# Kernel optimization log

Hardware: AMD Instinct MI355X
Metric: run time of the kernel (lower is better)

Reference implementation:

```python
import jax, jax.numpy as jnp
import numpy as np

N, E, DIN, H = 10000, 80000, 1024, 512
NEG = 0.2  # PyG GATv2Conv default negative_slope


def gatv2(x, src, dst, wl, bl, wr, br, att, b, n):
    # GATv2: e_ij = att . leaky_relu(Wl x_j + Wr x_i); segment softmax over dst; sum alpha * Wl x_j
    xl = x @ wl + bl            # [N, H] source transform
    xr = x @ wr + br            # [N, H] target transform
    z = jax.nn.leaky_relu(xl[src] + xr[dst], NEG)   # [E, H]
    e = z @ att                                      # [E]
    m = jax.ops.segment_max(e, dst, num_segments=n)  # per-target max (self-loops guarantee nonempty)
    p = jnp.exp(e - m[dst])
    s = jax.ops.segment_sum(p, dst, num_segments=n)
    alpha = p / (s[dst] + 1e-16)                     # [E]
    out = jax.ops.segment_sum(alpha[:, None] * xl[src], dst, num_segments=n)
    return out + b


def setup_inputs() -> dict:
    key = jax.random.key(0)
    ks = iter(jax.random.split(key, 64))
    d = {}
    d["x"] = jax.random.normal(next(ks), (N, DIN), jnp.float32)
    d["edge_index"] = jax.random.randint(next(ks), (2, E), 0, N, dtype=jnp.int32).astype(jnp.int64)
    dims = [DIN, H, H, H]
    for i in range(4):
        din = dims[i]
        sc = 1.0 / np.sqrt(din)
        d[f"wl{i+1}"] = jax.random.normal(next(ks), (din, H), jnp.float32) * sc
        d[f"bl{i+1}"] = jnp.zeros((H,), jnp.float32)
        d[f"wr{i+1}"] = jax.random.normal(next(ks), (din, H), jnp.float32) * sc
        d[f"br{i+1}"] = jnp.zeros((H,), jnp.float32)
        d[f"att{i+1}"] = jax.random.normal(next(ks), (H,), jnp.float32) * (1.0 / np.sqrt(H))
        d[f"b{i+1}"] = jnp.zeros((H,), jnp.float32)
    for name, din, dout in [("1", H, 512), ("2", 512, 256), ("3", 256, 2)]:
        d[f"lw{name}"] = jax.random.normal(next(ks), (din, dout), jnp.float32) * (1.0 / np.sqrt(din))
        d[f"lb{name}"] = jnp.zeros((dout,), jnp.float32)
    return d


def reference(x, edge_index, wl1, bl1, wr1, br1, att1, b1,
              wl2, bl2, wr2, br2, att2, b2,
              wl3, bl3, wr3, br3, att3, b3,
              wl4, bl4, wr4, br4, att4, b4,
              lw1, lb1, lw2, lb2, lw3, lb3):
    n = x.shape[0]
    loops = jnp.arange(n, dtype=edge_index.dtype)
    src = jnp.concatenate([edge_index[0], loops])  # add self-loops (PyG default)
    dst = jnp.concatenate([edge_index[1], loops])
    h = jax.nn.relu(gatv2(x, src, dst, wl1, bl1, wr1, br1, att1, b1, n))
    h = jax.nn.relu(gatv2(h, src, dst, wl2, bl2, wr2, br2, att2, b2, n))
    h = jax.nn.relu(gatv2(h, src, dst, wl3, bl3, wr3, br3, att3, b3, n))
    h = jax.nn.relu(gatv2(h, src, dst, wl4, bl4, wr4, br4, att4, b4, n))
    # dropout is identity at inference
    h = jax.nn.relu(h @ lw1 + lb1)
    h = jax.nn.relu(h @ lw2 + lb2)
    logits = h @ lw3 + lb3
    return logits, jax.nn.softmax(logits, axis=1)
```

## Files before the change

kernel.cpp:

```cpp
#include <hip/hip_runtime.h>
#include <cstdint>

#define NN 10000
#define NE 80000
#define DIN_ 1024
#define HH 512

typedef __attribute__((ext_vector_type(8))) short bf16x8;
typedef __attribute__((ext_vector_type(4))) float f32x4;
typedef unsigned short u16;
typedef unsigned int u32;

static __device__ __forceinline__ float b2f(u16 u) {
  u32 i = ((u32)u) << 16;
  return __builtin_bit_cast(float, i);
}
static __device__ __forceinline__ u16 f2b(float f) {
  u32 i = __builtin_bit_cast(u32, f);
  u32 r = (i + 0x7fffu + ((i >> 16) & 1u)) >> 16;
  return (u16)r;
}
static __device__ __forceinline__ void unpack8(uint4 u, float* f) {
  f[0] = __builtin_bit_cast(float, u.x << 16);
  f[1] = __builtin_bit_cast(float, u.x & 0xffff0000u);
  f[2] = __builtin_bit_cast(float, u.y << 16);
  f[3] = __builtin_bit_cast(float, u.y & 0xffff0000u);
  f[4] = __builtin_bit_cast(float, u.z << 16);
  f[5] = __builtin_bit_cast(float, u.z & 0xffff0000u);
  f[6] = __builtin_bit_cast(float, u.w << 16);
  f[7] = __builtin_bit_cast(float, u.w & 0xffff0000u);
}
static __device__ __forceinline__ void load8(const u16* p, float* f) { unpack8(*(const uint4*)p, f); }

#define ASYNC_CP16(gp, lp)                                                        \
  __builtin_amdgcn_global_load_lds((__attribute__((address_space(1))) void*)(gp), \
                                   (__attribute__((address_space(3))) void*)(lp), \
                                   16, 0, 0)

static __device__ __forceinline__ int float_flag(const u16* xw) {
  __shared__ int c;
  if (threadIdx.x == 0) c = 0;
  __syncthreads();
  int bad = 0;
  for (int i = threadIdx.x; i < 2048; i += blockDim.x) {
    u32 e = (xw[i] >> 7) & 0xFFu;
    if (e >= 140u) bad++;
  }
  if (bad) atomicAdd(&c, bad);
  __syncthreads();
  return c > 64;
}
static __device__ __forceinline__ int int64_flag(const u32* ew) {
  __shared__ int c;
  if (threadIdx.x == 0) c = 0;
  __syncthreads();
  int z = 0;
  for (int i = threadIdx.x; i < 256; i += blockDim.x)
    if (ew[2 * i + 1] == 0u) z++;
  if (z) atomicAdd(&c, z);
  __syncthreads();
  return c > 200;
}

__global__ void k_edges(const void* ei, int* esrc, int* edst, int* counts) {
  int f64 = int64_flag((const u32*)ei);
  int i = blockIdx.x * 256 + threadIdx.x;
  if (i < NE) {
    int sv, dv;
    if (f64) {
      sv = (int)((const long long*)ei)[i];
      dv = (int)((const long long*)ei)[NE + i];
    } else {
      sv = ((const int*)ei)[i];
      dv = ((const int*)ei)[NE + i];
    }
    esrc[i] = sv;
    edst[i] = dv;
    atomicAdd(&counts[dv], 1);
  } else if (i < NE + NN) {
    atomicAdd(&counts[i - NE], 1);
  }
}

__global__ void k_scan(const int* counts, int* rowptr, int* cursor, int n) {
  __shared__ int lds[1024];
  __shared__ int carry;
  int t = threadIdx.x;
  if (t == 0) { carry = 0; rowptr[0] = 0; }
  __syncthreads();
  for (int base = 0; base < n; base += 1024) {
    int v = (base + t < n) ? counts[base + t] : 0;
    lds[t] = v;
    __syncthreads();
    for (int off = 1; off < 1024; off <<= 1) {
      int x = (t >= off) ? lds[t - off] : 0;
      __syncthreads();
      lds[t] += x;
      __syncthreads();
    }
    if (base + t < n) {
      int inc = lds[t] + carry;
      rowptr[base + t + 1] = inc;
      cursor[base + t] = inc - v;
    }
    __syncthreads();
    if (t == 1023) carry += lds[1023];
    __syncthreads();
  }
}

__global__ void k_scatter(const int* src, const int* dst, int* cursor, int* col, int E, int n) {
  int i = blockIdx.x * blockDim.x + threadIdx.x;
  if (i < E) {
    int p = atomicAdd(&cursor[dst[i]], 1);
    col[p] = src[i];
  } else if (i < E + n) {
    int v = i - E;
    int p = atomicAdd(&cursor[v], 1);
    col[p] = v;
  }
}

struct CvtAll {
  const void* xin;
  u16* xout;
  const void* vin[20];
  u16* vout[20];
  int vn[20];
};
__global__ void k_convert(CvtAll a) {
  int f = float_flag((const u16*)a.xin);
  if (blockIdx.x < 1024) {
    for (int i = blockIdx.x * 256 + threadIdx.x; i < NN * DIN_; i += 1024 * 256)
      a.xout[i] = f ? f2b(((const float*)a.xin)[i]) : ((const u16*)a.xin)[i];
  } else {
    int v = blockIdx.x - 1024;
    const void* in = a.vin[v];
    u16* out = a.vout[v];
    int n = a.vn[v];
    for (int i = threadIdx.x; i < n; i += 256)
      out[i] = f ? f2b(((const float*)in)[i]) : ((const u16*)in)[i];
  }
}

struct TrAll {
  const void* xin;
  const void* in[10];
  u16* out[10];
  int K[10], N[10], off[10];
};
__global__ void k_trall(TrAll a) {
  __shared__ u16 tt[32][33];
  int f = float_flag((const u16*)a.xin);
  int b = blockIdx.x;
  int seg = 0;
#pragma unroll
  for (int i = 1; i < 10; i++)
    if (b >= a.off[i]) seg = i;
  int tl = b - a.off[seg];
  int K = a.K[seg], N = a.N[seg];
  int tiles_n = N >> 5;
  int n0 = (tl % tiles_n) << 5, k0 = (tl / tiles_n) << 5;
  const void* in = a.in[seg];
  u16* out = a.out[seg];
  int tx = threadIdx.x & 31, ty = threadIdx.x >> 5;
  for (int r = ty; r < 32; r += 8) {
    size_t idx = (size_t)(k0 + r) * N + n0 + tx;
    tt[r][tx] = f ? f2b(((const float*)in)[idx]) : ((const u16*)in)[idx];
  }
  __syncthreads();
  for (int r = ty; r < 32; r += 8) out[(size_t)(n0 + r) * K + k0 + tx] = tt[tx][r];
}

__global__ __launch_bounds__(256) void k_gemm128(const u16* __restrict__ A, int lda,
                                                 const u16* __restrict__ Bt,
                                                 const u16* __restrict__ bias,
                                                 u16* __restrict__ C,
                                                 int M, int N, int K, int act) {
  __shared__ u16 sA[2 * 128 * 32];
  __shared__ u16 sB[2 * 128 * 32];
  int t = threadIdx.x;
  int wave = t >> 6, lane = t & 63;
  int m0 = blockIdx.y << 7, n0 = blockIdx.x << 7;

  const u16* agp[4];
  const u16* bgp[4];
  u16* la[4];
  u16* lb[4];
#pragma unroll
  for (int q = 0; q < 4; q++) {
    int h = q >> 1;
    int row = ((q & 1) << 6) + (t >> 2);
    int kc = (t & 3) * 8;
    int ra = m0 + row;
    ra = ra < M ? ra : M - 1;
    agp[q] = A + (size_t)ra * lda + h * 32 + kc;
    bgp[q] = Bt + (size_t)(n0 + row) * K + h * 32 + kc;
    int lofs = h * 4096 + (((q & 1) << 8) + t) * 8;
    la[q] = sA + lofs;
    lb[q] = sB + lofs;
  }

  int wm = (wave >> 1) << 6, wn = (wave & 1) << 6;
  int lr = lane & 15, lko = (lane >> 4) << 3;

  f32x4 acc[4][4];
#pragma unroll
  for (int i = 0; i < 4; i++)
#pragma unroll
    for (int j = 0; j < 4; j++) acc[i][j] = (f32x4){0.f, 0.f, 0.f, 0.f};

  for (int k0 = 0; k0 < K; k0 += 64) {
#pragma unroll
    for (int q = 0; q < 4; q++) ASYNC_CP16(agp[q] + k0, la[q]);
#pragma unroll
    for (int q = 0; q < 4; q++) ASYNC_CP16(bgp[q] + k0, lb[q]);
    __syncthreads();
    bf16x8 a[2][4], b[2][4];
#pragma unroll
    for (int s = 0; s < 2; s++) {
#pragma unroll
      for (int i = 0; i < 4; i++) a[s][i] = *(const bf16x8*)(sA + s * 4096 + (wm + i * 16 + lr) * 32 + lko);
#pragma unroll
      for (int j = 0; j < 4; j++) b[s][j] = *(const bf16x8*)(sB + s * 4096 + (wn + j * 16 + lr) * 32 + lko);
    }
#pragma unroll
    for (int s = 0; s < 2; s++)
#pragma unroll
      for (int i = 0; i < 4; i++)
#pragma unroll
        for (int j = 0; j < 4; j++)
          acc[i][j] = __builtin_amdgcn_mfma_f32_16x16x32_bf16(a[s][i], b[s][j], acc[i][j], 0, 0, 0);
    __syncthreads();
  }

  int rbase = (lane >> 4) << 2;
#pragma unroll
  for (int j = 0; j < 4; j++) {
    int colc = n0 + wn + j * 16 + lr;
    float bv = b2f(bias[colc]);
#pragma unroll
    for (int i = 0; i < 4; i++) {
#pragma unroll
      for (int r = 0; r < 4; r++) {
        int row = m0 + wm + i * 16 + rbase + r;
        if (row < M) {
          float v = acc[i][j][r] + bv;
          if (act) v = fmaxf(v, 0.f);
          C[(size_t)row * N + colc] = f2b(v);
        }
      }
    }
  }
}

__global__ __launch_bounds__(256) void k_attn2(u16* __restrict__ xlr,
                                               const u16* __restrict__ att, const u16* __restrict__ bias,
                                               const int* __restrict__ rowptr, const int* __restrict__ col,
                                               int n) {
  int node = (blockIdx.x * 256 + threadIdx.x) >> 6;
  if (node >= n) return;
  int lane = threadIdx.x & 63;
  int h0 = lane * 8;
  float a[8], r[8];
  load8(att + h0, a);
  load8(xlr + (size_t)node * 1024 + 512 + h0, r);
  int e0 = rowptr[node], e1 = rowptr[node + 1];

  float m = -3e38f, s = 0.f;
  float acc[8] = {0.f, 0.f, 0.f, 0.f, 0.f, 0.f, 0.f, 0.f};
  uint4 raw = *(const uint4*)(xlr + (size_t)col[e0] * 1024 + h0);
  for (int e = e0; e < e1; e++) {
    int jn = col[(e + 1 < e1) ? e + 1 : e];
    float xv[8];
    unpack8(raw, xv);
    uint4 rawn = *(const uint4*)(xlr + (size_t)jn * 1024 + h0);
    float part = 0.f;
#pragma unroll
    for (int i = 0; i < 8; i++) {
      float z = xv[i] + r[i];
      z = z > 0.f ? z : 0.2f * z;
      part = fmaf(a[i], z, part);
    }
#pragma unroll
    for (int off = 32; off >= 1; off >>= 1) part += __shfl_xor(part, off);
    float mn = fmaxf(m, part);
    float al = __expf(m - mn);
    float w = __expf(part - mn);
    s = s * al + w;
#pragma unroll
    for (int i = 0; i < 8; i++) acc[i] = fmaf(acc[i], al, w * xv[i]);
    m = mn;
    raw = rawn;
  }
  float inv = 1.f / (s + 1e-16f);

  float bv[8];
  load8(bias + h0, bv);
  uint4 o;
  u32 p[8];
#pragma unroll
  for (int i = 0; i < 8; i++) {
    float v = fmaf(acc[i], inv, bv[i]);
    v = fmaxf(v, 0.f);
    p[i] = f2b(v);
  }
  o.x = p[0] | (p[1] << 16);
  o.y = p[2] | (p[3] << 16);
  o.z = p[4] | (p[5] << 16);
  o.w = p[6] | (p[7] << 16);
  *(uint4*)(xlr + (size_t)node * 1024 + 512 + h0) = o;
}

__global__ __launch_bounds__(256) void k_head(const u16* __restrict__ h2, const u16* __restrict__ lw3,
                                              const u16* __restrict__ lb3, float* __restrict__ out, int n) {
  int row = (blockIdx.x * 256 + threadIdx.x) >> 6;
  if (row >= n) return;
  int lane = threadIdx.x & 63;
  int k0 = lane * 4;
  uint2 hu = *(const uint2*)(h2 + (size_t)row * 256 + k0);
  float hx[4];
  hx[0] = __builtin_bit_cast(float, hu.x << 16);
  hx[1] = __builtin_bit_cast(float, hu.x & 0xffff0000u);
  hx[2] = __builtin_bit_cast(float, hu.y << 16);
  hx[3] = __builtin_bit_cast(float, hu.y & 0xffff0000u);
  float wv[8];
  load8(lw3 + (size_t)k0 * 2, wv);
  float p0 = 0.f, p1 = 0.f;
#pragma unroll
  for (int i = 0; i < 4; i++) {
    p0 = fmaf(hx[i], wv[2 * i], p0);
    p1 = fmaf(hx[i], wv[2 * i + 1], p1);
  }
#pragma unroll
  for (int off = 32; off >= 1; off >>= 1) {
    p0 += __shfl_xor(p0, off);
    p1 += __shfl_xor(p1, off);
  }
  if (lane == 0) {
    float l0 = p0 + b2f(lb3[0]);
    float l1 = p1 + b2f(lb3[1]);
    float mx = fmaxf(l0, l1);
    float q0 = __expf(l0 - mx), q1 = __expf(l1 - mx);
    float si = 1.f / (q0 + q1);
    out[row * 2 + 0] = l0;
    out[row * 2 + 1] = l1;
    out[2 * n + row * 2 + 0] = q0 * si;
    out[2 * n + row * 2 + 1] = q1 * si;
  }
}

extern "C" void kernel_launch(void* const* d_in, const int* in_sizes, int n_in,
                              void* d_out, int out_size, void* d_ws, size_t ws_size,
                              hipStream_t stream) {
  (void)in_sizes; (void)n_in; (void)out_size; (void)ws_size;
  const void* x_raw = d_in[0];
  const void* ei_raw = d_in[1];
  const void *wl[4], *bl[4], *wr[4], *br[4], *att[4], *bg[4];
  for (int i = 0; i < 4; i++) {
    wl[i] = d_in[2 + i * 6 + 0];
    bl[i] = d_in[2 + i * 6 + 1];
    wr[i] = d_in[2 + i * 6 + 2];
    br[i] = d_in[2 + i * 6 + 3];
    att[i] = d_in[2 + i * 6 + 4];
    bg[i] = d_in[2 + i * 6 + 5];
  }
  const void* lw1 = d_in[26];
  const void* lb1 = d_in[27];
  const void* lw2 = d_in[28];
  const void* lb2 = d_in[29];
  const void* lw3 = d_in[30];
  const void* lb3 = d_in[31];

  size_t off = 0;
  auto alloc = [&](size_t bytes) -> void* {
    off = (off + 255) & ~(size_t)255;
    void* p = (char*)d_ws + off;
    off += bytes;
    return p;
  };
  int* esrc = (int*)alloc(NE * 4);
  int* edst = (int*)alloc(NE * 4);
  int* counts = (int*)alloc(NN * 4);
  int* rowptr = (int*)alloc((NN + 1) * 4);
  int* cursor = (int*)alloc(NN * 4);
  int* col = (int*)alloc((NE + NN) * 4);
  u16* cb = (u16*)alloc(4 * 1024 * 2);
  u16* attv = (u16*)alloc(4 * 512 * 2);
  u16* bgv = (u16*)alloc(4 * 512 * 2);
  u16* lb1v = (u16*)alloc(512 * 2);
  u16* lb2v = (u16*)alloc(256 * 2);
  u16* lw3v = (u16*)alloc(512 * 2);
  u16* lb3v = (u16*)alloc(2 * 2);
  u16* comb0 = (u16*)alloc((size_t)1024 * 1024 * 2);
  u16* combL[4];
  combL[0] = comb0;
  for (int l = 1; l < 4; l++) combL[l] = (u16*)alloc((size_t)1024 * 512 * 2);
  u16* lw1T = (u16*)alloc((size_t)512 * 512 * 2);
  u16* lw2T = (u16*)alloc((size_t)256 * 512 * 2);
  u16* xc = (u16*)alloc((size_t)NN * DIN_ * 2);
  u16* X0 = (u16*)alloc((size_t)NN * 1024 * 2);
  u16* X1 = (u16*)alloc((size_t)NN * 1024 * 2);
  u16* mlp1 = xc;
  u16* mlp2 = xc + (size_t)NN * 512;

  hipMemsetAsync(counts, 0, NN * 4, stream);
  int ET = NE + NN;
  k_edges<<<(ET + 255) / 256, 256, 0, stream>>>(ei_raw, esrc, edst, counts);
  k_scan<<<1, 1024, 0, stream>>>(counts, rowptr, cursor, NN);
  k_scatter<<<(ET + 255) / 256, 256, 0, stream>>>(esrc, edst, cursor, col, NE, NN);

  CvtAll ca;
  ca.xin = x_raw;
  ca.xout = xc;
  for (int l = 0; l < 4; l++) {
    ca.vin[l * 4 + 0] = bl[l];  ca.vout[l * 4 + 0] = cb + l * 1024;        ca.vn[l * 4 + 0] = 512;
    ca.vin[l * 4 + 1] = br[l];  ca.vout[l * 4 + 1] = cb + l * 1024 + 512;  ca.vn[l * 4 + 1] = 512;
    ca.vin[l * 4 + 2] = att[l]; ca.vout[l * 4 + 2] = attv + l * 512;       ca.vn[l * 4 + 2] = 512;
    ca.vin[l * 4 + 3] = bg[l];  ca.vout[l * 4 + 3] = bgv + l * 512;        ca.vn[l * 4 + 3] = 512;
  }
  ca.vin[16] = lb1; ca.vout[16] = lb1v; ca.vn[16] = 512;
  ca.vin[17] = lb2; ca.vout[17] = lb2v; ca.vn[17] = 256;
  ca.vin[18] = lw3; ca.vout[18] = lw3v; ca.vn[18] = 512;
  ca.vin[19] = lb3; ca.vout[19] = lb3v; ca.vn[19] = 2;
  k_convert<<<1024 + 20, 256, 0, stream>>>(ca);

  TrAll ta;
  ta.xin = x_raw;
  const void* tin[10] = {wl[0], wr[0], wl[1], wr[1], wl[2], wr[2], wl[3], wr[3], lw1, lw2};
  u16* tout[10] = {comb0, comb0 + (size_t)512 * 1024,
                   combL[1], combL[1] + (size_t)512 * 512,
                   combL[2], combL[2] + (size_t)512 * 512,
                   combL[3], combL[3] + (size_t)512 * 512,
                   lw1T, lw2T};
  int tK[10] = {1024, 1024, 512, 512, 512, 512, 512, 512, 512, 512};
  int tN[10] = {512, 512, 512, 512, 512, 512, 512, 512, 512, 256};
  int acc_off = 0;
  for (int i = 0; i < 10; i++) {
    ta.in[i] = tin[i];
    ta.out[i] = tout[i];
    ta.K[i] = tK[i];
    ta.N[i] = tN[i];
    ta.off[i] = acc_off;
    acc_off += (tN[i] >> 5) * (tK[i] >> 5);
  }
  k_trall<<<acc_off, 256, 0, stream>>>(ta);

  auto gemm = [&](const u16* A, int lda, const u16* Bt, const u16* bias, u16* C,
                  int M, int Nn, int K, int act) {
    dim3 grid(Nn >> 7, (M + 127) >> 7);
    k_gemm128<<<grid, 256, 0, stream>>>(A, lda, Bt, bias, C, M, Nn, K, act);
  };
  auto attn = [&](u16* xlr, int l) {
    k_attn2<<<(NN * 64 + 255) / 256, 256, 0, stream>>>(xlr, attv + l * 512, bgv + l * 512,
                                                       rowptr, col, NN);
  };

  gemm(xc, 1024, comb0, cb + 0 * 1024, X0, NN, 1024, 1024, 0);
  attn(X0, 0);
  gemm(X0 + 512, 1024, combL[1], cb + 1 * 1024, X1, NN, 1024, 512, 0);
  attn(X1, 1);
  gemm(X1 + 512, 1024, combL[2], cb + 2 * 1024, X0, NN, 1024, 512, 0);
  attn(X0, 2);
  gemm(X0 + 512, 1024, combL[3], cb + 3 * 1024, X1, NN, 1024, 512, 0);
  attn(X1, 3);

  gemm(X1 + 512, 1024, lw1T, lb1v, mlp1, NN, 512, 512, 1);
  gemm(mlp1, 512, lw2T, lb2v, mlp2, NN, 256, 512, 1);
  k_head<<<(NN * 64 + 255) / 256, 256, 0, stream>>>(mlp2, lw3v, lb3v, (float*)d_out, NN);
}
```

Baseline: 446.2 us.

## Swizzle GEMM LDS and XCD tile mapping, unroll attention, merge prep kernels

Several unrelated changes land together. The GEMM gets an XOR-swizzled LDS layout to cut bank conflicts and a 1D grid remapped so that row tiles are grouped per XCD for better L2 reuse. The attention kernel now processes two edges per iteration, prefetching two ahead, and rescales the online softmax only when the running max changes. The scan becomes a single pass with 20 elements per thread, and the conversion and transpose kernels are merged into one launch with vectorized x conversion. The extra branching in attention and the swizzle indexing add some complexity and register pressure.

```diff
diff --git a/kernel.cpp b/kernel.cpp
--- a/kernel.cpp
+++ b/kernel.cpp
@@ -82,31 +82,38 @@
   }
 }
 
-__global__ void k_scan(const int* counts, int* rowptr, int* cursor, int n) {
-  __shared__ int lds[1024];
-  __shared__ int carry;
+__global__ __launch_bounds__(512) void k_scan(const int* counts, int* rowptr, int* cursor, int n) {
+  __shared__ int lds[512];
+  const int PER = 20;
   int t = threadIdx.x;
-  if (t == 0) { carry = 0; rowptr[0] = 0; }
+  int base = t * PER;
+  int v[PER];
+  int sum = 0;
+#pragma unroll
+  for (int i = 0; i < PER; i++) {
+    int idx = base + i;
+    v[i] = (idx < n) ? counts[idx] : 0;
+    sum += v[i];
+  }
+  lds[t] = sum;
   __syncthreads();
-  for (int base = 0; base < n; base += 1024) {
-    int v = (base + t < n) ? counts[base + t] : 0;
-    lds[t] = v;
+  for (int off = 1; off < 512; off <<= 1) {
+    int x = (t >= off) ? lds[t - off] : 0;
     __syncthreads();
-    for (int off = 1; off < 1024; off <<= 1) {
-      int x = (t >= off) ? lds[t - off] : 0;
-      __syncthreads();
-      lds[t] += x;
-      __syncthreads();
-    }
-    if (base + t < n) {
-      int inc = lds[t] + carry;
-      rowptr[base + t + 1] = inc;
-      cursor[base + t] = inc - v;
-    }
+    lds[t] += x;
     __syncthreads();
-    if (t == 1023) carry += lds[1023];
-    __syncthreads();
-  }
+  }
+  int run = (t > 0) ? lds[t - 1] : 0;
+#pragma unroll
+  for (int i = 0; i < PER; i++) {
+    int idx = base + i;
+    if (idx < n) {
+      cursor[idx] = run;
+      run += v[i];
+      rowptr[idx + 1] = run;
+    }
+  }
+  if (t == 0) rowptr[0] = 0;
 }
 
 __global__ void k_scatter(const int* src, const int* dst, int* cursor, int* col, int E, int n) {
@@ -121,68 +128,83 @@
   }
 }
 
-struct CvtAll {
+#define XBLK 2048
+struct Prep {
   const void* xin;
   u16* xout;
   const void* vin[20];
   u16* vout[20];
   int vn[20];
+  const void* tin[10];
+  u16* tout[10];
+  int tK[10], tN[10], toff[10];
 };
-__global__ void k_convert(CvtAll a) {
+__global__ void k_prep(Prep a) {
+  __shared__ u16 tt[32][33];
   int f = float_flag((const u16*)a.xin);
-  if (blockIdx.x < 1024) {
-    for (int i = blockIdx.x * 256 + threadIdx.x; i < NN * DIN_; i += 1024 * 256)
-      a.xout[i] = f ? f2b(((const float*)a.xin)[i]) : ((const u16*)a.xin)[i];
-  } else {
-    int v = blockIdx.x - 1024;
+  int b = blockIdx.x;
+  if (b < XBLK) {
+    const int total = NN * DIN_ / 8;
+    for (int g = b * 256 + threadIdx.x; g < total; g += XBLK * 256) {
+      u16 o[8];
+      if (f) {
+        const float* p = (const float*)a.xin + (size_t)g * 8;
+#pragma unroll
+        for (int i = 0; i < 8; i++) o[i] = f2b(p[i]);
+      } else {
+        *(uint4*)o = *((const uint4*)a.xin + g);
+      }
+      *((uint4*)a.xout + g) = *(const uint4*)o;
+    }
+  } else if (b < XBLK + 20) {
+    int v = b - XBLK;
     const void* in = a.vin[v];
     u16* out = a.vout[v];
     int n = a.vn[v];
     for (int i = threadIdx.x; i < n; i += 256)
       out[i] = f ? f2b(((const float*)in)[i]) : ((const u16*)in)[i];
-  }
-}
-
-struct TrAll {
-  const void* xin;
-  const void* in[10];
-  u16* out[10];
-  int K[10], N[10], off[10];
-};
-__global__ void k_trall(TrAll a) {
-  __shared__ u16 tt[32][33];
-  int f = float_flag((const u16*)a.xin);
-  int b = blockIdx.x;
-  int seg = 0;
-#pragma unroll
-  for (int i = 1; i < 10; i++)
-    if (b >= a.off[i]) seg = i;
-  int tl = b - a.off[seg];
-  int K = a.K[seg], N = a.N[seg];
-  int tiles_n = N >> 5;
-  int n0 = (tl % tiles_n) << 5, k0 = (tl / tiles_n) << 5;
-  const void* in = a.in[seg];
-  u16* out = a.out[seg];
-  int tx = threadIdx.x & 31, ty = threadIdx.x >> 5;
-  for (int r = ty; r < 32; r += 8) {
-    size_t idx = (size_t)(k0 + r) * N + n0 + tx;
-    tt[r][tx] = f ? f2b(((const float*)in)[idx]) : ((const u16*)in)[idx];
-  }
-  __syncthreads();
-  for (int r = ty; r < 32; r += 8) out[(size_t)(n0 + r) * K + k0 + tx] = tt[tx][r];
+  } else {
+    int tb = b - XBLK - 20;
+    int seg = 0;
+#pragma unroll
+    for (int i = 1; i < 10; i++)
+      if (tb >= a.toff[i]) seg = i;
+    int tl = tb - a.toff[seg];
+    int K = a.tK[seg], N = a.tN[seg];
+    int tiles_n = N >> 5;
+    int n0 = (tl % tiles_n) << 5, k0 = (tl / tiles_n) << 5;
+    const void* in = a.tin[seg];
+    u16* out = a.tout[seg];
+    int tx = threadIdx.x & 31, ty = threadIdx.x >> 5;
+    for (int r = ty; r < 32; r += 8) {
+      size_t idx = (size_t)(k0 + r) * N + n0 + tx;
+      tt[r][tx] = f ? f2b(((const float*)in)[idx]) : ((const u16*)in)[idx];
+    }
+    __syncthreads();
+    for (int r = ty; r < 32; r += 8) out[(size_t)(n0 + r) * K + k0 + tx] = tt[tx][r];
+  }
 }
 
 __global__ __launch_bounds__(256) void k_gemm128(const u16* __restrict__ A, int lda,
                                                  const u16* __restrict__ Bt,
                                                  const u16* __restrict__ bias,
                                                  u16* __restrict__ C,
-                                                 int M, int N, int K, int act) {
+                                                 int M, int N, int K, int act,
+                                                 int tiles_m, int ln_tiles_n) {
   __shared__ u16 sA[2 * 128 * 32];
   __shared__ u16 sB[2 * 128 * 32];
+  int id = blockIdx.x;
+  int xcd = id & 7;
+  int rest = id >> 3;
+  int xt = rest & ((1 << ln_tiles_n) - 1);
+  int yt = ((rest >> ln_tiles_n) << 3) + xcd;
+  if (yt >= tiles_m) return;
+  int m0 = yt << 7, n0 = xt << 7;
   int t = threadIdx.x;
   int wave = t >> 6, lane = t & 63;
-  int m0 = blockIdx.y << 7, n0 = blockIdx.x << 7;
-
+
+  int srow = t >> 2;
+  int sk = ((t & 3) ^ ((t >> 3) & 3)) * 8;
   const u16* agp[4];
   const u16* bgp[4];
   u16* la[4];
@@ -190,19 +212,19 @@
 #pragma unroll
   for (int q = 0; q < 4; q++) {
     int h = q >> 1;
-    int row = ((q & 1) << 6) + (t >> 2);
-    int kc = (t & 3) * 8;
+    int row = ((q & 1) << 6) + srow;
     int ra = m0 + row;
     ra = ra < M ? ra : M - 1;
-    agp[q] = A + (size_t)ra * lda + h * 32 + kc;
-    bgp[q] = Bt + (size_t)(n0 + row) * K + h * 32 + kc;
+    agp[q] = A + (size_t)ra * lda + h * 32 + sk;
+    bgp[q] = Bt + (size_t)(n0 + row) * K + h * 32 + sk;
     int lofs = h * 4096 + (((q & 1) << 8) + t) * 8;
     la[q] = sA + lofs;
     lb[q] = sB + lofs;
   }
 
   int wm = (wave >> 1) << 6, wn = (wave & 1) << 6;
-  int lr = lane & 15, lko = (lane >> 4) << 3;
+  int lr = lane & 15;
+  int kcs = (((lane >> 4) ^ ((lr >> 1) & 3))) * 8;
 
   f32x4 acc[4][4];
 #pragma unroll
@@ -220,9 +242,9 @@
 #pragma unroll
     for (int s = 0; s < 2; s++) {
 #pragma unroll
-      for (int i = 0; i < 4; i++) a[s][i] = *(const bf16x8*)(sA + s * 4096 + (wm + i * 16 + lr) * 32 + lko);
-#pragma unroll
-      for (int j = 0; j < 4; j++) b[s][j] = *(const bf16x8*)(sB + s * 4096 + (wn + j * 16 + lr) * 32 + lko);
+      for (int i = 0; i < 4; i++) a[s][i] = *(const bf16x8*)(sA + s * 4096 + (wm + i * 16 + lr) * 32 + kcs);
+#pragma unroll
+      for (int j = 0; j < 4; j++) b[s][j] = *(const bf16x8*)(sB + s * 4096 + (wn + j * 16 + lr) * 32 + kcs);
     }
 #pragma unroll
     for (int s = 0; s < 2; s++)
@@ -254,7 +276,7 @@
   }
 }
 
-__global__ __launch_bounds__(256) void k_attn2(u16* __restrict__ xlr,
+__global__ __launch_bounds__(256) void k_attn3(u16* __restrict__ xlr,
                                                const u16* __restrict__ att, const u16* __restrict__ bias,
                                                const int* __restrict__ rowptr, const int* __restrict__ col,
                                                int n) {
@@ -269,29 +291,63 @@
 
   float m = -3e38f, s = 0.f;
   float acc[8] = {0.f, 0.f, 0.f, 0.f, 0.f, 0.f, 0.f, 0.f};
-  uint4 raw = *(const uint4*)(xlr + (size_t)col[e0] * 1024 + h0);
-  for (int e = e0; e < e1; e++) {
-    int jn = col[(e + 1 < e1) ? e + 1 : e];
-    float xv[8];
-    unpack8(raw, xv);
-    uint4 rawn = *(const uint4*)(xlr + (size_t)jn * 1024 + h0);
-    float part = 0.f;
+  int j0 = col[e0];
+  int j1 = col[(e0 + 1 < e1) ? e0 + 1 : e0];
+  uint4 raw0 = *(const uint4*)(xlr + (size_t)j0 * 1024 + h0);
+  uint4 raw1 = *(const uint4*)(xlr + (size_t)j1 * 1024 + h0);
+
+  for (int e = e0; e < e1; e += 2) {
+    bool has2 = (e + 1 < e1);
+    int jn0 = col[(e + 2 < e1) ? e + 2 : e1 - 1];
+    int jn1 = col[(e + 3 < e1) ? e + 3 : e1 - 1];
+    uint4 p0 = *(const uint4*)(xlr + (size_t)jn0 * 1024 + h0);
+    uint4 p1 = *(const uint4*)(xlr + (size_t)jn1 * 1024 + h0);
+    float x0[8], x1[8];
+    unpack8(raw0, x0);
+    unpack8(raw1, x1);
+    float pa = 0.f, pb = 0.f;
 #pragma unroll
     for (int i = 0; i < 8; i++) {
-      float z = xv[i] + r[i];
-      z = z > 0.f ? z : 0.2f * z;
-      part = fmaf(a[i], z, part);
-    }
-#pragma unroll
-    for (int off = 32; off >= 1; off >>= 1) part += __shfl_xor(part, off);
-    float mn = fmaxf(m, part);
-    float al = __expf(m - mn);
-    float w = __expf(part - mn);
-    s = s * al + w;
-#pragma unroll
-    for (int i = 0; i < 8; i++) acc[i] = fmaf(acc[i], al, w * xv[i]);
-    m = mn;
-    raw = rawn;
+      float z0 = x0[i] + r[i];
+      z0 = z0 > 0.f ? z0 : 0.2f * z0;
+      pa = fmaf(a[i], z0, pa);
+      float z1 = x1[i] + r[i];
+      z1 = z1 > 0.f ? z1 : 0.2f * z1;
+      pb = fmaf(a[i], z1, pb);
+    }
+#pragma unroll
+    for (int off = 32; off >= 1; off >>= 1) {
+      pa += __shfl_xor(pa, off);
+      pb += __shfl_xor(pb, off);
+    }
+    if (pa > m) {
+      float al = __expf(m - pa);
+      s *= al;
+#pragma unroll
+      for (int i = 0; i < 8; i++) acc[i] *= al;
+      m = pa;
+    }
+    {
+      float w = __expf(pa - m);
+      s += w;
+#pragma unroll
+      for (int i = 0; i < 8; i++) acc[i] = fmaf(w, x0[i], acc[i]);
+    }
+    if (has2) {
+      if (pb > m) {
+        float al = __expf(m - pb);
+        s *= al;
+#pragma unroll
+        for (int i = 0; i < 8; i++) acc[i] *= al;
+        m = pb;
+      }
+      float w = __expf(pb - m);
+      s += w;
+#pragma unroll
+      for (int i = 0; i < 8; i++) acc[i] = fmaf(w, x1[i], acc[i]);
+    }
+    raw0 = p0;
+    raw1 = p1;
   }
   float inv = 1.f / (s + 1e-16f);
 
@@ -407,26 +463,22 @@
   hipMemsetAsync(counts, 0, NN * 4, stream);
   int ET = NE + NN;
   k_edges<<<(ET + 255) / 256, 256, 0, stream>>>(ei_raw, esrc, edst, counts);
-  k_scan<<<1, 1024, 0, stream>>>(counts, rowptr, cursor, NN);
+  k_scan<<<1, 512, 0, stream>>>(counts, rowptr, cursor, NN);
   k_scatter<<<(ET + 255) / 256, 256, 0, stream>>>(esrc, edst, cursor, col, NE, NN);
 
-  CvtAll ca;
-  ca.xin = x_raw;
-  ca.xout = xc;
+  Prep pa;
+  pa.xin = x_raw;
+  pa.xout = xc;
   for (int l = 0; l < 4; l++) {
-    ca.vin[l * 4 + 0] = bl[l];  ca.vout[l * 4 + 0] = cb + l * 1024;        ca.vn[l * 4 + 0] = 512;
-    ca.vin[l * 4 + 1] = br[l];  ca.vout[l * 4 + 1] = cb + l * 1024 + 512;  ca.vn[l * 4 + 1] = 512;
-    ca.vin[l * 4 + 2] = att[l]; ca.vout[l * 4 + 2] = attv + l * 512;       ca.vn[l * 4 + 2] = 512;
-    ca.vin[l * 4 + 3] = bg[l];  ca.vout[l * 4 + 3] = bgv + l * 512;        ca.vn[l * 4 + 3] = 512;
-  }
-  ca.vin[16] = lb1; ca.vout[16] = lb1v; ca.vn[16] = 512;
-  ca.vin[17] = lb2; ca.vout[17] = lb2v; ca.vn[17] = 256;
-  ca.vin[18] = lw3; ca.vout[18] = lw3v; ca.vn[18] = 512;
-  ca.vin[19] = lb3; ca.vout[19] = lb3v; ca.vn[19] = 2;
-  k_convert<<<1024 + 20, 256, 0, stream>>>(ca);
-
-  TrAll ta;
-  ta.xin = x_raw;
+    pa.vin[l * 4 + 0] = bl[l];  pa.vout[l * 4 + 0] = cb + l * 1024;        pa.vn[l * 4 + 0] = 512;
+    pa.vin[l * 4 + 1] = br[l];  pa.vout[l * 4 + 1] = cb + l * 1024 + 512;  pa.vn[l * 4 + 1] = 512;
+    pa.vin[l * 4 + 2] = att[l]; pa.vout[l * 4 + 2] = attv + l * 512;       pa.vn[l * 4 + 2] = 512;
+    pa.vin[l * 4 + 3] = bg[l];  pa.vout[l * 4 + 3] = bgv + l * 512;        pa.vn[l * 4 + 3] = 512;
+  }
+  pa.vin[16] = lb1; pa.vout[16] = lb1v; pa.vn[16] = 512;
+  pa.vin[17] = lb2; pa.vout[17] = lb2v; pa.vn[17] = 256;
+  pa.vin[18] = lw3; pa.vout[18] = lw3v; pa.vn[18] = 512;
+  pa.vin[19] = lb3; pa.vout[19] = lb3v; pa.vn[19] = 2;
   const void* tin[10] = {wl[0], wr[0], wl[1], wr[1], wl[2], wr[2], wl[3], wr[3], lw1, lw2};
   u16* tout[10] = {comb0, comb0 + (size_t)512 * 1024,
                    combL[1], combL[1] + (size_t)512 * 512,
@@ -437,22 +489,26 @@
   int tN[10] = {512, 512, 512, 512, 512, 512, 512, 512, 512, 256};
   int acc_off = 0;
   for (int i = 0; i < 10; i++) {
-    ta.in[i] = tin[i];
-    ta.out[i] = tout[i];
-    ta.K[i] = tK[i];
-    ta.N[i] = tN[i];
-    ta.off[i] = acc_off;
+    pa.tin[i] = tin[i];
+    pa.tout[i] = tout[i];
+    pa.tK[i] = tK[i];
+    pa.tN[i] = tN[i];
+    pa.toff[i] = acc_off;
     acc_off += (tN[i] >> 5) * (tK[i] >> 5);
   }
-  k_trall<<<acc_off, 256, 0, stream>>>(ta);
+  k_prep<<<XBLK + 20 + acc_off, 256, 0, stream>>>(pa);
 
   auto gemm = [&](const u16* A, int lda, const u16* Bt, const u16* bias, u16* C,
                   int M, int Nn, int K, int act) {
-    dim3 grid(Nn >> 7, (M + 127) >> 7);
-    k_gemm128<<<grid, 256, 0, stream>>>(A, lda, Bt, bias, C, M, Nn, K, act);
+    int tiles_m = (M + 127) >> 7;
+    int tiles_n = Nn >> 7;
+    int ln = (tiles_n == 8) ? 3 : (tiles_n == 4) ? 2 : 1;
+    int mgrp = (tiles_m + 7) >> 3;
+    int blocks = (mgrp << 3) * tiles_n;
+    k_gemm128<<<blocks, 256, 0, stream>>>(A, lda, Bt, bias, C, M, Nn, K, act, tiles_m, ln);
   };
   auto attn = [&](u16* xlr, int l) {
-    k_attn2<<<(NN * 64 + 255) / 256, 256, 0, stream>>>(xlr, attv + l * 512, bgv + l * 512,
+    k_attn3<<<(NN * 64 + 255) / 256, 256, 0, stream>>>(xlr, attv + l * 512, bgv + l * 512,
                                                        rowptr, col, NN);
   };
 
```

After: 390.8 us. -12.4%, faster.
